# Performance work log

Measured on AMD Instinct MI355X. Metric: run time of the kernel, lower is better.

Reference implementation:

```python
import jax, jax.numpy as jnp
import numpy as np

B, S, H = 2, 2048, 1024
NUM_HEADS = 16
HEAD_DIM = H // NUM_HEADS  # 64
SCALE = HEAD_DIM ** -0.5


def apply_rope(x, cos, sin):
    # x: [B, nh, S, hd]; cos/sin: [1, 1, S, hd//2]
    x1 = x[..., ::2]
    x2 = x[..., 1::2]
    rotated = jnp.stack([x1 * cos - x2 * sin, x1 * sin + x2 * cos], axis=-1)
    return rotated.reshape(x.shape)


def setup_inputs() -> dict:
    key = jax.random.key(0)
    ks = jax.random.split(key, 7)
    return {
        "x": jax.random.normal(ks[0], (B, S, H), dtype=jnp.float32),
        "cos": jax.random.normal(ks[1], (S, HEAD_DIM // 2), dtype=jnp.float32),
        "sin": jax.random.normal(ks[2], (S, HEAD_DIM // 2), dtype=jnp.float32),
        "wq": jax.random.normal(ks[3], (H, H), dtype=jnp.float32) * (H ** -0.5),
        "wk": jax.random.normal(ks[4], (H, H), dtype=jnp.float32) * (H ** -0.5),
        "wv": jax.random.normal(ks[5], (H, H), dtype=jnp.float32) * (H ** -0.5),
        "wo": jax.random.normal(ks[6], (H, H), dtype=jnp.float32) * (H ** -0.5),
    }


def reference(x, cos, sin, wq, wk, wv, wo):
    b, s, h = x.shape
    nh, hd = NUM_HEADS, HEAD_DIM
    # torch Linear: y = x @ W.T
    q = (x @ wq.T).reshape(b, s, nh, hd).transpose(0, 2, 1, 3)  # [b, nh, s, hd]
    k = (x @ wk.T).reshape(b, s, nh, hd).transpose(0, 2, 1, 3)
    v = (x @ wv.T).reshape(b, s, nh, hd).transpose(0, 2, 1, 3)

    c = cos[None, None]  # [1,1,s,hd//2]
    sn = sin[None, None]
    q = apply_rope(q, c, sn)
    k = apply_rope(k, c, sn)

    scores = jnp.einsum("bhqd,bhkd->bhqk", q, k) * SCALE  # [b, nh, s, s]
    causal_mask = jnp.triu(jnp.ones((s, s), dtype=bool), k=1)
    scores = jnp.where(causal_mask[None, None], -jnp.inf, scores)
    attn = jax.nn.softmax(scores, axis=-1)
    out = jnp.einsum("bhqk,bhkd->bhqd", attn, v)  # [b, nh, s, hd]
    out = out.transpose(0, 2, 1, 3).reshape(b, s, h)
    return out @ wo.T
```

## Files before the change

kernel.cpp:

```cpp
#include <hip/hip_runtime.h>

typedef __attribute__((ext_vector_type(8))) __bf16 bf16x8;
typedef __attribute__((ext_vector_type(4))) float f32x4;
typedef __attribute__((ext_vector_type(4))) unsigned short ushort4v;

__device__ __forceinline__ unsigned short f2bf(float x) {
  union { float f; unsigned u; } v; v.f = x;
  unsigned r = v.u + 0x7fffu + ((v.u >> 16) & 1u);
  return (unsigned short)(r >> 16);
}

#define GLDS16(g, l) __builtin_amdgcn_global_load_lds( \
    (__attribute__((address_space(1))) void*)(g), \
    (__attribute__((address_space(3))) void*)(l), 16, 0, 0)

__global__ void cvt_f32_bf16(const float* __restrict__ src,
                             unsigned short* __restrict__ dst, int n4) {
  int i = blockIdx.x * blockDim.x + threadIdx.x;
  if (i >= n4) return;
  float4 v = reinterpret_cast<const float4*>(src)[i];
  ushort4v o;
  o.x = f2bf(v.x); o.y = f2bf(v.y); o.z = f2bf(v.z); o.w = f2bf(v.w);
  reinterpret_cast<ushort4v*>(dst)[i] = o;
}

template <int MODE>
__global__ __launch_bounds__(256) void gemm_bt(
    const unsigned short* __restrict__ A, const unsigned short* __restrict__ Bw,
    const float* __restrict__ cosT, const float* __restrict__ sinT,
    unsigned short* __restrict__ Qh, unsigned short* __restrict__ Kh,
    unsigned short* __restrict__ Vt, float* __restrict__ outF) {
  __shared__ __align__(16) unsigned char smA[2][8192];
  __shared__ __align__(16) unsigned char smB[2][8192];
  const int t = threadIdx.x;
  const int lane = t & 63, wvi = t >> 6;
  const int wr = wvi >> 1, wc = wvi & 1;
  const int g = lane >> 4, li = lane & 15;
  const int row0 = blockIdx.y * 128, col0 = blockIdx.x * 128;

  const int schunk = (t & 3) ^ ((t >> 2) & 3);
  const size_t arow = (size_t)(row0 + (t >> 2)) * 1024 + schunk * 8;
  const size_t brow = (size_t)(col0 + (t >> 2)) * 1024 + schunk * 8;

  f32x4 acc[4][4];
#pragma unroll
  for (int mi = 0; mi < 4; ++mi)
#pragma unroll
    for (int ni = 0; ni < 4; ++ni) acc[mi][ni] = (f32x4){0.f, 0.f, 0.f, 0.f};

  auto stage = [&](int buf, int k0) {
    GLDS16(A + arow + k0, &smA[buf][t * 16]);
    GLDS16(A + arow + 64 * 1024 + k0, &smA[buf][4096 + t * 16]);
    GLDS16(Bw + brow + k0, &smB[buf][t * 16]);
    GLDS16(Bw + brow + 64 * 1024 + k0, &smB[buf][4096 + t * 16]);
  };

  stage(0, 0);
  for (int kk = 0; kk < 32; ++kk) {
    __syncthreads();
    const int buf = kk & 1;
    if (kk < 31) stage(buf ^ 1, (kk + 1) * 32);
    bf16x8 af[4], bfr[4];
#pragma unroll
    for (int mi = 0; mi < 4; ++mi)
      af[mi] = *reinterpret_cast<const bf16x8*>(
          &smA[buf][((wr * 64 + mi * 16 + li) << 6) + ((g ^ (li & 3)) << 4)]);
#pragma unroll
    for (int ni = 0; ni < 4; ++ni)
      bfr[ni] = *reinterpret_cast<const bf16x8*>(
          &smB[buf][((wc * 64 + ni * 16 + li) << 6) + ((g ^ (li & 3)) << 4)]);
#pragma unroll
    for (int mi = 0; mi < 4; ++mi)
#pragma unroll
      for (int ni = 0; ni < 4; ++ni)
        acc[mi][ni] = __builtin_amdgcn_mfma_f32_16x16x32_bf16(
            af[mi], bfr[ni], acc[mi][ni], 0, 0, 0);
  }

#pragma unroll
  for (int mi = 0; mi < 4; ++mi) {
    const int rowb = row0 + wr * 64 + mi * 16 + g * 4;
#pragma unroll
    for (int ni = 0; ni < 4; ++ni) {
      const int col = col0 + wc * 64 + ni * 16 + li;
#pragma unroll
      for (int r = 0; r < 4; ++r) {
        float v = acc[mi][ni][r];
        const int rr = rowb + r;
        if (MODE == 1) {
          outF[(size_t)rr * 1024 + col] = v;
        } else {
          const int s = rr & 2047, b = rr >> 11;
          const int jj = col & 1023;
          const int h = jj >> 6, d = jj & 63;
          const int bh = b * 16 + h;
          const int typ = col >> 10;
          if (typ == 2) {
            Vt[((size_t)bh * 64 + d) * 2048 + s] = f2bf(v);
          } else {
            const float cs = cosT[s * 32 + (d >> 1)];
            const float sn = sinT[s * 32 + (d >> 1)];
            const float pr = __shfl_xor(v, 1);
            float rv = (d & 1) ? (pr * sn + v * cs) : (v * cs - pr * sn);
            if (typ == 0) rv *= 0.18033688011112042f;
            unsigned short* dst = (typ == 0) ? Qh : Kh;
            dst[((size_t)bh * 2048 + s) * 64 + d] = f2bf(rv);
          }
        }
      }
    }
  }
}

__global__ __launch_bounds__(256, 4) void attn_fwd(
    const unsigned short* __restrict__ Qh, const unsigned short* __restrict__ Kh,
    const unsigned short* __restrict__ Vt, unsigned short* __restrict__ Ob) {
  __shared__ __align__(16) unsigned short Plds[4][16][72];

  const int t = threadIdx.x, lane = t & 63, w = t >> 6;
  const int g = lane >> 4, li = lane & 15;
  const int bh = blockIdx.x, qt = blockIdx.y;
  const int q0 = qt * 64;

  const unsigned short* __restrict__ Kbh = Kh + (size_t)bh * 2048 * 64;
  const unsigned short* __restrict__ Vbh = Vt + (size_t)bh * 64 * 2048;

  bf16x8 qa[2];
  {
    const unsigned short* qrow =
        Qh + ((size_t)bh * 2048 + q0 + w * 16 + li) * 64 + g * 8;
    qa[0] = *reinterpret_cast<const bf16x8*>(qrow);
    qa[1] = *reinterpret_cast<const bf16x8*>(qrow + 32);
  }

  float m_[4], l_[4];
  f32x4 oacc[4];
#pragma unroll
  for (int r = 0; r < 4; ++r) { m_[r] = -1e30f; l_[r] = 0.f; }
#pragma unroll
  for (int dt = 0; dt < 4; ++dt) oacc[dt] = (f32x4){0.f, 0.f, 0.f, 0.f};

  for (int kt = 0; kt <= qt; ++kt) {
    const int kv0 = kt * 64;

    f32x4 sacc[4];
#pragma unroll
    for (int ct = 0; ct < 4; ++ct) {
      const unsigned short* krow = Kbh + (size_t)(kv0 + ct * 16 + li) * 64 + g * 8;
      bf16x8 kb0 = *reinterpret_cast<const bf16x8*>(krow);
      bf16x8 kb1 = *reinterpret_cast<const bf16x8*>(krow + 32);
      f32x4 z = (f32x4){0.f, 0.f, 0.f, 0.f};
      z = __builtin_amdgcn_mfma_f32_16x16x32_bf16(qa[0], kb0, z, 0, 0, 0);
      z = __builtin_amdgcn_mfma_f32_16x16x32_bf16(qa[1], kb1, z, 0, 0, 0);
      sacc[ct] = z;
    }

    bf16x8 vb[8];
#pragma unroll
    for (int dt = 0; dt < 4; ++dt) {
      const unsigned short* vrow = Vbh + (size_t)(dt * 16 + li) * 2048 + kv0 + g * 8;
      vb[2 * dt] = *reinterpret_cast<const bf16x8*>(vrow);
      vb[2 * dt + 1] = *reinterpret_cast<const bf16x8*>(vrow + 32);
    }

    if (kt == qt) {
#pragma unroll
      for (int ct = 0; ct < 4; ++ct)
#pragma unroll
        for (int r = 0; r < 4; ++r)
          if (ct * 16 + li > w * 16 + g * 4 + r) sacc[ct][r] = -1e30f;
    }

    float mnew[4], alpha[4], psum[4];
#pragma unroll
    for (int r = 0; r < 4; ++r) {
      float tm = fmaxf(fmaxf(sacc[0][r], sacc[1][r]), fmaxf(sacc[2][r], sacc[3][r]));
      tm = fmaxf(tm, __shfl_xor(tm, 1));
      tm = fmaxf(tm, __shfl_xor(tm, 2));
      tm = fmaxf(tm, __shfl_xor(tm, 4));
      tm = fmaxf(tm, __shfl_xor(tm, 8));
      const float mn = fmaxf(m_[r], tm);
      mnew[r] = mn;
      alpha[r] = __builtin_amdgcn_exp2f(m_[r] - mn);
      m_[r] = mn;
      psum[r] = 0.f;
    }
#pragma unroll
    for (int ct = 0; ct < 4; ++ct)
#pragma unroll
      for (int r = 0; r < 4; ++r) {
        const float p = __builtin_amdgcn_exp2f(sacc[ct][r] - mnew[r]);
        psum[r] += p;
        Plds[w][g * 4 + r][ct * 16 + li] = f2bf(p);
      }
#pragma unroll
    for (int r = 0; r < 4; ++r) {
      float ps = psum[r];
      ps += __shfl_xor(ps, 1);
      ps += __shfl_xor(ps, 2);
      ps += __shfl_xor(ps, 4);
      ps += __shfl_xor(ps, 8);
      l_[r] = l_[r] * alpha[r] + ps;
#pragma unroll
      for (int dt = 0; dt < 4; ++dt) oacc[dt][r] *= alpha[r];
    }
    __builtin_amdgcn_wave_barrier();
    bf16x8 pa0, pa1;
    __builtin_memcpy(&pa0, &Plds[w][li][g * 8], 16);
    __builtin_memcpy(&pa1, &Plds[w][li][32 + g * 8], 16);
    __builtin_amdgcn_sched_barrier(0);
#pragma unroll
    for (int dt = 0; dt < 4; ++dt) {
      oacc[dt] = __builtin_amdgcn_mfma_f32_16x16x32_bf16(pa0, vb[2 * dt], oacc[dt], 0, 0, 0);
      oacc[dt] = __builtin_amdgcn_mfma_f32_16x16x32_bf16(pa1, vb[2 * dt + 1], oacc[dt], 0, 0, 0);
    }
    __syncthreads();
  }

  const int b = bh >> 4, h = bh & 15;
#pragma unroll
  for (int r = 0; r < 4; ++r) {
    const float inv = 1.0f / l_[r];
    const int row = q0 + w * 16 + g * 4 + r;
#pragma unroll
    for (int dt = 0; dt < 4; ++dt)
      Ob[((size_t)b * 2048 + row) * 1024 + h * 64 + dt * 16 + li] =
          f2bf(oacc[dt][r] * inv);
  }
}

extern "C" void kernel_launch(void* const* d_in, const int* in_sizes, int n_in,
                              void* d_out, int out_size, void* d_ws, size_t ws_size,
                              hipStream_t stream) {
  const float* x = (const float*)d_in[0];
  const float* cosT = (const float*)d_in[1];
  const float* sinT = (const float*)d_in[2];
  const float* wq = (const float*)d_in[3];
  const float* wk = (const float*)d_in[4];
  const float* wv = (const float*)d_in[5];
  const float* wo = (const float*)d_in[6];
  float* out = (float*)d_out;

  char* ws = (char*)d_ws;
  unsigned short* xb    = (unsigned short*)(ws);
  unsigned short* wqkvb = (unsigned short*)(ws + 8388608);
  unsigned short* wob   = (unsigned short*)(ws + 14680064);
  unsigned short* Qh    = (unsigned short*)(ws + 16777216);
  unsigned short* Kh    = (unsigned short*)(ws + 25165824);
  unsigned short* Vt    = (unsigned short*)(ws + 33554432);
  unsigned short* Ob    = (unsigned short*)(ws + 41943040);

  cvt_f32_bf16<<<4096, 256, 0, stream>>>(x, xb, 1048576);
  cvt_f32_bf16<<<1024, 256, 0, stream>>>(wq, wqkvb, 262144);
  cvt_f32_bf16<<<1024, 256, 0, stream>>>(wk, wqkvb + 1048576, 262144);
  cvt_f32_bf16<<<1024, 256, 0, stream>>>(wv, wqkvb + 2097152, 262144);
  cvt_f32_bf16<<<1024, 256, 0, stream>>>(wo, wob, 262144);

  gemm_bt<0><<<dim3(24, 32), 256, 0, stream>>>(xb, wqkvb, cosT, sinT, Qh, Kh, Vt,
                                               nullptr);
  attn_fwd<<<dim3(32, 32), 256, 0, stream>>>(Qh, Kh, Vt, Ob);
  gemm_bt<1><<<dim3(8, 32), 256, 0, stream>>>(Ob, wob, nullptr, nullptr, nullptr,
                                              nullptr, nullptr, out);
}
```

Baseline: 324.5 us.

## Pair causal query tiles per block and drop per-iteration block barrier

Each attention block now holds 8 waves that handle two query tiles, y and 31-y. This evens out causal work across blocks and halves the grid. The P staging buffer is double-buffered by iteration parity, which lets the __syncthreads at the end of each key tile be removed. The per-tile row-sum shuffle reduction is deferred to the epilogue, since l can be rescaled per lane. The risks are higher register pressure from launch_bounds(512,4) and whether the wave barrier alone is enough to order the LDS accesses within each wave.

Result: faster. 307.4 us (-5.3%).

```diff
diff --git a/kernel.cpp b/kernel.cpp
--- a/kernel.cpp
+++ b/kernel.cpp
@@ -112,14 +112,16 @@
   }
 }
 
-__global__ __launch_bounds__(256, 4) void attn_fwd(
+__global__ __launch_bounds__(512, 4) void attn_fwd(
     const unsigned short* __restrict__ Qh, const unsigned short* __restrict__ Kh,
     const unsigned short* __restrict__ Vt, unsigned short* __restrict__ Ob) {
-  __shared__ __align__(16) unsigned short Plds[4][16][72];
+  __shared__ __align__(16) unsigned short Plds[2][8][16][72];
 
   const int t = threadIdx.x, lane = t & 63, w = t >> 6;
+  const int wg = w >> 2, wl = w & 3;
   const int g = lane >> 4, li = lane & 15;
-  const int bh = blockIdx.x, qt = blockIdx.y;
+  const int bh = blockIdx.x, y = blockIdx.y;
+  const int qt = wg ? (31 - y) : y;
   const int q0 = qt * 64;
 
   const unsigned short* __restrict__ Kbh = Kh + (size_t)bh * 2048 * 64;
@@ -128,7 +130,7 @@
   bf16x8 qa[2];
   {
     const unsigned short* qrow =
-        Qh + ((size_t)bh * 2048 + q0 + w * 16 + li) * 64 + g * 8;
+        Qh + ((size_t)bh * 2048 + q0 + wl * 16 + li) * 64 + g * 8;
     qa[0] = *reinterpret_cast<const bf16x8*>(qrow);
     qa[1] = *reinterpret_cast<const bf16x8*>(qrow + 32);
   }
@@ -142,6 +144,7 @@
 
   for (int kt = 0; kt <= qt; ++kt) {
     const int kv0 = kt * 64;
+    const int par = kt & 1;
 
     f32x4 sacc[4];
 #pragma unroll
@@ -168,10 +171,10 @@
       for (int ct = 0; ct < 4; ++ct)
 #pragma unroll
         for (int r = 0; r < 4; ++r)
-          if (ct * 16 + li > w * 16 + g * 4 + r) sacc[ct][r] = -1e30f;
-    }
-
-    float mnew[4], alpha[4], psum[4];
+          if (ct * 16 + li > wl * 16 + g * 4 + r) sacc[ct][r] = -1e30f;
+    }
+
+    float mnew[4], alpha[4];
 #pragma unroll
     for (int r = 0; r < 4; ++r) {
       float tm = fmaxf(fmaxf(sacc[0][r], sacc[1][r]), fmaxf(sacc[2][r], sacc[3][r]));
@@ -183,45 +186,42 @@
       mnew[r] = mn;
       alpha[r] = __builtin_amdgcn_exp2f(m_[r] - mn);
       m_[r] = mn;
-      psum[r] = 0.f;
-    }
-#pragma unroll
-    for (int ct = 0; ct < 4; ++ct)
-#pragma unroll
-      for (int r = 0; r < 4; ++r) {
+    }
+#pragma unroll
+    for (int r = 0; r < 4; ++r) {
+      float ps = 0.f;
+#pragma unroll
+      for (int ct = 0; ct < 4; ++ct) {
         const float p = __builtin_amdgcn_exp2f(sacc[ct][r] - mnew[r]);
-        psum[r] += p;
-        Plds[w][g * 4 + r][ct * 16 + li] = f2bf(p);
+        ps += p;
+        Plds[par][w][g * 4 + r][ct * 16 + li] = f2bf(p);
       }
-#pragma unroll
-    for (int r = 0; r < 4; ++r) {
-      float ps = psum[r];
-      ps += __shfl_xor(ps, 1);
-      ps += __shfl_xor(ps, 2);
-      ps += __shfl_xor(ps, 4);
-      ps += __shfl_xor(ps, 8);
       l_[r] = l_[r] * alpha[r] + ps;
 #pragma unroll
       for (int dt = 0; dt < 4; ++dt) oacc[dt][r] *= alpha[r];
     }
     __builtin_amdgcn_wave_barrier();
     bf16x8 pa0, pa1;
-    __builtin_memcpy(&pa0, &Plds[w][li][g * 8], 16);
-    __builtin_memcpy(&pa1, &Plds[w][li][32 + g * 8], 16);
+    __builtin_memcpy(&pa0, &Plds[par][w][li][g * 8], 16);
+    __builtin_memcpy(&pa1, &Plds[par][w][li][32 + g * 8], 16);
     __builtin_amdgcn_sched_barrier(0);
 #pragma unroll
     for (int dt = 0; dt < 4; ++dt) {
       oacc[dt] = __builtin_amdgcn_mfma_f32_16x16x32_bf16(pa0, vb[2 * dt], oacc[dt], 0, 0, 0);
       oacc[dt] = __builtin_amdgcn_mfma_f32_16x16x32_bf16(pa1, vb[2 * dt + 1], oacc[dt], 0, 0, 0);
     }
-    __syncthreads();
   }
 
   const int b = bh >> 4, h = bh & 15;
 #pragma unroll
   for (int r = 0; r < 4; ++r) {
-    const float inv = 1.0f / l_[r];
-    const int row = q0 + w * 16 + g * 4 + r;
+    float ls = l_[r];
+    ls += __shfl_xor(ls, 1);
+    ls += __shfl_xor(ls, 2);
+    ls += __shfl_xor(ls, 4);
+    ls += __shfl_xor(ls, 8);
+    const float inv = 1.0f / ls;
+    const int row = q0 + wl * 16 + g * 4 + r;
 #pragma unroll
     for (int dt = 0; dt < 4; ++dt)
       Ob[((size_t)b * 2048 + row) * 1024 + h * 64 + dt * 16 + li] =
@@ -258,7 +258,7 @@
 
   gemm_bt<0><<<dim3(24, 32), 256, 0, stream>>>(xb, wqkvb, cosT, sinT, Qh, Kh, Vt,
                                                nullptr);
-  attn_fwd<<<dim3(32, 32), 256, 0, stream>>>(Qh, Kh, Vt, Ob);
+  attn_fwd<<<dim3(32, 16), 512, 0, stream>>>(Qh, Kh, Vt, Ob);
   gemm_bt<1><<<dim3(8, 32), 256, 0, stream>>>(Ob, wob, nullptr, nullptr, nullptr,
                                               nullptr, nullptr, out);
 }
```
